# Kernel tuning notes

Hardware: AMD Instinct MI355X
Metric: run time of the kernel (lower is better)

## Reference

```python
import jax, jax.numpy as jnp
import numpy as np

H = 384
W = 384
C_X = 64       # channels of x (== out_channels)
C_PTX = 64     # channels of ptx
C_IN = C_X + C_PTX  # Linear in_channels = 128
C_OUT = 64
N_TGT = 120000  # number of target pixels (CSR segments)
DEG = 8         # points per target pixel
N_PTS = N_TGT * DEG


def setup_inputs() -> dict:
    key = jax.random.key(0)
    k1, k2, k3, k4 = jax.random.split(key, 4)
    x = jax.random.normal(k1, (1, C_X, H, W), jnp.float32)
    ptx = jax.random.normal(k2, (N_PTS, C_PTX), jnp.float32)
    # CSR row pointer over points per target pixel (monotone, ends at N_PTS)
    point_key = jnp.arange(N_TGT + 1, dtype=jnp.int32) * DEG
    # unique target-pixel indices into H*W
    pixel_tgt_idx = jnp.arange(N_TGT, dtype=jnp.int32)
    sm_w = jax.random.normal(k3, (C_IN, 1), jnp.float32) * 0.05
    sm_b = jnp.zeros((1,), jnp.float32)
    fo_w = jax.random.normal(k4, (C_IN, C_OUT), jnp.float32) * 0.05
    fo_b = jnp.zeros((C_OUT,), jnp.float32)
    return {"x": x, "ptx": ptx, "sm_w": sm_w, "sm_b": sm_b,
            "fo_w": fo_w, "fo_b": fo_b, "point_key": point_key,
            "pixel_tgt_idx": pixel_tgt_idx, "bs": 1, "height": H, "width": W}


def reference(x, ptx, sm_w, sm_b, fo_w, fo_b, point_key, pixel_tgt_idx, bs, height, width):
    # segment id per point from CSR rowptr (static total length for jit)
    seg = jnp.repeat(jnp.arange(N_TGT, dtype=jnp.int32), jnp.diff(point_key),
                     total_repeat_length=N_PTS)
    # pixel features gathered to target pixels, then CSR-gathered to points
    feat_px = x.transpose(0, 2, 3, 1).reshape(height * width, C_X)[pixel_tgt_idx]
    feat = jnp.concatenate([ptx, feat_px[seg]], axis=1)  # [N_PTS, C_IN]
    # _net_forward: identity (base class)
    # segment softmax over points within each pixel group
    logits = feat @ sm_w + sm_b  # [N_PTS, 1]
    m = jax.ops.segment_max(logits, seg, num_segments=N_TGT)
    e = jnp.exp(logits - m[seg])
    s = jax.ops.segment_sum(e, seg, num_segments=N_TGT)
    weight = e / (s[seg] + 1e-16)
    # feat_out projection replaces ptx
    ptx_out = feat @ fo_w + fo_b  # [N_PTS, C_OUT]
    agg = jax.ops.segment_sum(weight * ptx_out, seg, num_segments=N_TGT)  # [N_TGT, C_OUT]
    # list_to_map: scatter aggregated features back to image grid + mask
    flat = jnp.zeros((height * width, C_OUT), x.dtype).at[pixel_tgt_idx].set(agg)
    mask = jnp.zeros((height * width, 1), x.dtype).at[pixel_tgt_idx].set(1.0)
    fmap = flat.reshape(1, height, width, C_OUT).transpose(0, 3, 1, 2)
    mmap = mask.reshape(1, height, width, 1).transpose(0, 3, 1, 2)
    x_out = jnp.where(mmap > 0, fmap, x)
    return x_out, ptx_out
```

## Files before the change

### kernel.cpp

```cpp
#include <hip/hip_runtime.h>
#include <hip/hip_bf16.h>
#include <math.h>

typedef __attribute__((ext_vector_type(8))) short short8v;
typedef __attribute__((ext_vector_type(4))) float float4v;

#define TB 64

__device__ __forceinline__ short f2bf(float f) {
    __hip_bfloat16 h = __float2bfloat16(f);
    short s; __builtin_memcpy(&s, &h, sizeof(short));
    return s;
}
__device__ __forceinline__ float4v mfma_bf16(short8v a, short8v b, float4v c) {
    return __builtin_amdgcn_mfma_f32_16x16x32_bf16(a, b, c, 0, 0, 0);
}

__device__ __forceinline__ int WTI(int row, int col) {
    return row * 72 + (col ^ (((row >> 2) & 7) << 3));
}

__global__ __launch_bounds__(256)
void copy_x_kernel(const float4* __restrict__ x, float4* __restrict__ out, int n4) {
    int i = blockIdx.x * blockDim.x + threadIdx.x;
    if (i < n4) out[i] = x[i];
}

__global__ __launch_bounds__(256, 4)
void fused_kernel(const float* __restrict__ x,
                  const float* __restrict__ ptx,
                  const float* __restrict__ sm_w,
                  const float* __restrict__ fo_w,
                  const float* __restrict__ fo_b,
                  const int* __restrict__ point_key,
                  const int* __restrict__ pixel_tgt_idx,
                  float* __restrict__ xout,
                  float* __restrict__ ptx_out,
                  int n_tgt, int n_pts, int hw)
{
    __shared__ __align__(16) char sraw[34816];
    unsigned short (*fpx)[72] = (unsigned short (*)[72])sraw;
    unsigned short* wTf       = (unsigned short*)(sraw + 9216);
    float (*q_lds)[68]        = (float (*)[68])sraw;
    float (*agg)[68]          = (float (*)[68])(sraw + 17408);
    __shared__ int pix_s[TB], r0_s[TB], deg_s[TB];

    const int tid  = threadIdx.x;
    const int lane = tid & 63;
    const int w    = tid >> 6;
    const int lo16 = lane & 15;
    const int g    = lane >> 4;
    const int t0   = blockIdx.x * TB;
    const int tw0  = w * 16;

    float4 wv[8];
    {
        const float4* fw4 = (const float4*)fo_w;
        #pragma unroll
        for (int i = 0; i < 8; ++i) wv[i] = fw4[i * 256 + tid];
    }
    float4 fb40 = *(const float4*)&fo_b[ 0 + g * 4];
    float4 fb41 = *(const float4*)&fo_b[16 + g * 4];
    float4 fb42 = *(const float4*)&fo_b[32 + g * 4];
    float4 fb43 = *(const float4*)&fo_b[48 + g * 4];
    if (tid < TB) {
        int t = t0 + tid;
        bool v = t < n_tgt;
        int r0 = v ? point_key[t] : 0;
        int d  = v ? (point_key[t + 1] - r0) : 0;
        pix_s[tid] = v ? pixel_tgt_idx[t] : 0;
        r0_s[tid]  = r0;
        deg_s[tid] = d > 8 ? 8 : d;
    }

    #pragma unroll
    for (int i = 0; i < 8; ++i) {
        int flat = (i * 256 + tid) * 4;
        int k = flat >> 6, c = flat & 63;
        int wrow0 = (k & 64) + c;
        int col = k & 63;
        wTf[WTI(wrow0 + 0, col)] = (unsigned short)f2bf(wv[i].x);
        wTf[WTI(wrow0 + 1, col)] = (unsigned short)f2bf(wv[i].y);
        wTf[WTI(wrow0 + 2, col)] = (unsigned short)f2bf(wv[i].z);
        wTf[WTI(wrow0 + 3, col)] = (unsigned short)f2bf(wv[i].w);
    }
    __syncthreads();

    int pgm[8];
    #pragma unroll
    for (int mt = 0; mt < 8; ++mt) {
        int tlA = tw0 + mt * 2 + (lo16 >> 3);
        int pg  = r0_s[tlA] + (lo16 & 7);
        pgm[mt] = pg < n_pts ? pg : n_pts - 1;
    }

    {
        const int tgt = tid >> 2, q4 = tid & 3;
        const int pix = pix_s[tgt];
        const float* xp = x + (size_t)(q4 * 16) * hw + pix;
        #pragma unroll
        for (int hhalf = 0; hhalf < 2; ++hhalf) {
            short8v pk;
            #pragma unroll
            for (int j = 0; j < 8; ++j)
                pk[j] = f2bf(xp[(size_t)(hhalf * 8 + j) * hw]);
            *(short8v*)&fpx[tgt][q4 * 16 + hhalf * 8] = pk;
        }
    }

    short8v b1[5][2];
    #pragma unroll
    for (int ct = 0; ct < 4; ++ct)
        #pragma unroll
        for (int kh = 0; kh < 2; ++kh)
            b1[ct][kh] = *(const short8v*)&wTf[WTI(ct * 16 + lo16, kh * 32 + g * 8)];
    #pragma unroll
    for (int kh = 0; kh < 2; ++kh) {
        short8v bb;
        #pragma unroll
        for (int j = 0; j < 8; ++j)
            bb[j] = f2bf(sm_w[kh * 32 + g * 8 + j]);
        b1[4][kh] = bb;
    }

    float4 lb0, lb1, lb2, lb3;
    {
        const float* prow = ptx + (size_t)pgm[0] * 64 + g * 8;
        lb0 = *(const float4*)(prow);
        lb1 = *(const float4*)(prow + 4);
        lb2 = *(const float4*)(prow + 32);
        lb3 = *(const float4*)(prow + 36);
    }
    __syncthreads();

    float4v qv4[4];
    {
        short8v a20 = *(const short8v*)&fpx[tw0 + lo16][g * 8];
        short8v a21 = *(const short8v*)&fpx[tw0 + lo16][32 + g * 8];
        #pragma unroll
        for (int ct = 0; ct < 4; ++ct) {
            short8v b20 = *(const short8v*)&wTf[WTI(64 + ct * 16 + lo16, g * 8)];
            short8v b21 = *(const short8v*)&wTf[WTI(64 + ct * 16 + lo16, 32 + g * 8)];
            float4v z = {0.f, 0.f, 0.f, 0.f};
            z = mfma_bf16(b20, a20, z);
            qv4[ct] = mfma_bf16(b21, a21, z);
        }
    }
    __syncthreads();
    {
        float4v t0v = qv4[0]; t0v[0] += fb40.x; t0v[1] += fb40.y; t0v[2] += fb40.z; t0v[3] += fb40.w;
        float4v t1v = qv4[1]; t1v[0] += fb41.x; t1v[1] += fb41.y; t1v[2] += fb41.z; t1v[3] += fb41.w;
        float4v t2v = qv4[2]; t2v[0] += fb42.x; t2v[1] += fb42.y; t2v[2] += fb42.z; t2v[3] += fb42.w;
        float4v t3v = qv4[3]; t3v[0] += fb43.x; t3v[1] += fb43.y; t3v[2] += fb43.z; t3v[3] += fb43.w;
        *(float4v*)&q_lds[tw0 + lo16][ 0 + g * 4] = t0v;
        *(float4v*)&q_lds[tw0 + lo16][16 + g * 4] = t1v;
        *(float4v*)&q_lds[tw0 + lo16][32 + g * 4] = t2v;
        *(float4v*)&q_lds[tw0 + lo16][48 + g * 4] = t3v;
    }

#define EPIL_CT(CT, CREG)                                                      \
    {                                                                          \
        const int colb = (CT) * 16 + g * 4;                                    \
        const float4 q4 = *(const float4*)&q_lds[tE][colb];                    \
        float4v po;                                                            \
        po[0] = CREG[0] + q4.x; po[1] = CREG[1] + q4.y;                        \
        po[2] = CREG[2] + q4.z; po[3] = CREG[3] + q4.w;                        \
        if (val)                                                               \
            *(float4v*)&ptx_out[(size_t)(r0E + pE) * 64 + colb] = po;          \
        float s0 = po[0] * wn, s1 = po[1] * wn, s2 = po[2] * wn, s3 = po[3] * wn; \
        s0 += __shfl_xor(s0, 1); s1 += __shfl_xor(s1, 1);                      \
        s2 += __shfl_xor(s2, 1); s3 += __shfl_xor(s3, 1);                      \
        s0 += __shfl_xor(s0, 2); s1 += __shfl_xor(s1, 2);                      \
        s2 += __shfl_xor(s2, 2); s3 += __shfl_xor(s3, 2);                      \
        s0 += __shfl_xor(s0, 4); s1 += __shfl_xor(s1, 4);                      \
        s2 += __shfl_xor(s2, 4); s3 += __shfl_xor(s3, 4);                      \
        if (pE == 0) {                                                         \
            float4v ag; ag[0] = s0; ag[1] = s1; ag[2] = s2; ag[3] = s3;        \
            *(float4v*)&agg[tE][colb] = ag;                                    \
        }                                                                      \
    }

    #pragma unroll
    for (int mt = 0; mt < 8; ++mt) {
        short8v a0, a1;
        a0[0] = f2bf(lb0.x); a0[1] = f2bf(lb0.y); a0[2] = f2bf(lb0.z); a0[3] = f2bf(lb0.w);
        a0[4] = f2bf(lb1.x); a0[5] = f2bf(lb1.y); a0[6] = f2bf(lb1.z); a0[7] = f2bf(lb1.w);
        a1[0] = f2bf(lb2.x); a1[1] = f2bf(lb2.y); a1[2] = f2bf(lb2.z); a1[3] = f2bf(lb2.w);
        a1[4] = f2bf(lb3.x); a1[5] = f2bf(lb3.y); a1[6] = f2bf(lb3.z); a1[7] = f2bf(lb3.w);

        if (mt < 7) {
            const float* prow = ptx + (size_t)pgm[mt + 1] * 64 + g * 8;
            lb0 = *(const float4*)(prow);
            lb1 = *(const float4*)(prow + 4);
            lb2 = *(const float4*)(prow + 32);
            lb3 = *(const float4*)(prow + 36);
        }

        float4v z = {0.f, 0.f, 0.f, 0.f};
        float4v cc0 = mfma_bf16(b1[0][1], a1, mfma_bf16(b1[0][0], a0, z));
        float4v cc1 = mfma_bf16(b1[1][1], a1, mfma_bf16(b1[1][0], a0, z));
        float4v cc2 = mfma_bf16(b1[2][1], a1, mfma_bf16(b1[2][0], a0, z));
        float4v cc3 = mfma_bf16(b1[3][1], a1, mfma_bf16(b1[3][0], a0, z));
        float4v cc4 = mfma_bf16(b1[4][1], a1, mfma_bf16(b1[4][0], a0, z));

        const int tE   = tw0 + mt * 2 + (lo16 >> 3);
        const int degE = deg_s[tE];
        const int r0E  = r0_s[tE];
        const int pE   = lo16 & 7;
        const bool val = (pE < degE);

        float lg = val ? cc4[0] : -3.4e38f;
        float mx = lg;
        mx = fmaxf(mx, __shfl_xor(mx, 1));
        mx = fmaxf(mx, __shfl_xor(mx, 2));
        mx = fmaxf(mx, __shfl_xor(mx, 4));
        float e = val ? __expf(lg - mx) : 0.0f;
        float sm = e;
        sm += __shfl_xor(sm, 1);
        sm += __shfl_xor(sm, 2);
        sm += __shfl_xor(sm, 4);
        const float wn = e / (sm + 1e-16f);

        EPIL_CT(0, cc0)
        EPIL_CT(1, cc1)
        EPIL_CT(2, cc2)
        EPIL_CT(3, cc3)
    }
#undef EPIL_CT
    __syncthreads();

    {
        const int tgt = tid >> 2, q4 = tid & 3;
        if (t0 + tgt < n_tgt) {
            const int pix = pix_s[tgt];
            float* xp = xout + (size_t)(q4 * 16) * hw + pix;
            #pragma unroll
            for (int u = 0; u < 4; ++u) {
                float4 v = *(const float4*)&agg[tgt][q4 * 16 + u * 4];
                xp[(size_t)(u * 4 + 0) * hw] = v.x;
                xp[(size_t)(u * 4 + 1) * hw] = v.y;
                xp[(size_t)(u * 4 + 2) * hw] = v.z;
                xp[(size_t)(u * 4 + 3) * hw] = v.w;
            }
        }
    }
}

extern "C" void kernel_launch(void* const* d_in, const int* in_sizes, int n_in,
                              void* d_out, int out_size, void* d_ws, size_t ws_size,
                              hipStream_t stream) {
    const float* x             = (const float*)d_in[0];
    const float* ptx           = (const float*)d_in[1];
    const float* sm_w          = (const float*)d_in[2];
    const float* fo_w          = (const float*)d_in[4];
    const float* fo_b          = (const float*)d_in[5];
    const int*   point_key     = (const int*)d_in[6];
    const int*   pixel_tgt_idx = (const int*)d_in[7];

    const int x_elems = in_sizes[0];
    const int hw      = x_elems / 64;
    const int n_tgt   = in_sizes[7];
    const int n_pts   = in_sizes[1] / 64;

    float* xout    = (float*)d_out;
    float* ptx_out = xout + (size_t)x_elems;

    const int n4 = x_elems / 4;
    copy_x_kernel<<<(n4 + 255) / 256, 256, 0, stream>>>(
        (const float4*)x, (float4*)xout, n4);

    const int blocks = (n_tgt + TB - 1) / TB;
    fused_kernel<<<blocks, 256, 0, stream>>>(
        x, ptx, sm_w, fo_w, fo_b, point_key, pixel_tgt_idx,
        xout, ptx_out, n_tgt, n_pts, hw);
}
```

Baseline: 137.0 us.

## Skip copying masked x pixels, store q in bf16 LDS, deepen ptx prefetch

Builds a per-pixel byte mask of target pixels in workspace and copies only the groups of four pixels that are not fully covered by targets, so x rows overwritten by the fused kernel are not copied. The per-target q projection is stored in LDS as bf16 instead of fp32, which shrinks shared memory enough to raise launch bounds to 5 blocks per CU. The ptx row prefetch becomes two-deep. The bf16 q adds rounding error to ptx_out, and the extra memset and mask launches add fixed overhead.

New measurement: 254.0 us. 1.85x slower.

```diff
diff --git a/kernel.cpp b/kernel.cpp
--- a/kernel.cpp
+++ b/kernel.cpp
@@ -3,6 +3,7 @@
 #include <math.h>
 
 typedef __attribute__((ext_vector_type(8))) short short8v;
+typedef __attribute__((ext_vector_type(4))) short short4v;
 typedef __attribute__((ext_vector_type(4))) float float4v;
 
 #define TB 64
@@ -12,12 +13,33 @@
     short s; __builtin_memcpy(&s, &h, sizeof(short));
     return s;
 }
+__device__ __forceinline__ float bf2f(short u) {
+    unsigned int x = ((unsigned int)(unsigned short)u) << 16;
+    float f; __builtin_memcpy(&f, &x, sizeof(float));
+    return f;
+}
 __device__ __forceinline__ float4v mfma_bf16(short8v a, short8v b, float4v c) {
     return __builtin_amdgcn_mfma_f32_16x16x32_bf16(a, b, c, 0, 0, 0);
 }
 
 __device__ __forceinline__ int WTI(int row, int col) {
     return row * 72 + (col ^ (((row >> 2) & 7) << 3));
+}
+
+__global__ __launch_bounds__(256)
+void mask_set_kernel(const int* __restrict__ idx, unsigned char* __restrict__ mask, int n) {
+    int i = blockIdx.x * blockDim.x + threadIdx.x;
+    if (i < n) mask[idx[i]] = 1;
+}
+
+__global__ __launch_bounds__(256)
+void copy_masked_kernel(const float4* __restrict__ x, float4* __restrict__ out,
+                        const unsigned int* __restrict__ mask4, int q4n) {
+    int q = blockIdx.x * blockDim.x + threadIdx.x;
+    if (q >= q4n) return;
+    if (mask4[q] == 0x01010101u) return;
+    size_t idx = (size_t)blockIdx.y * q4n + q;
+    out[idx] = x[idx];
 }
 
 __global__ __launch_bounds__(256)
@@ -26,7 +48,7 @@
     if (i < n4) out[i] = x[i];
 }
 
-__global__ __launch_bounds__(256, 4)
+__global__ __launch_bounds__(256, 5)
 void fused_kernel(const float* __restrict__ x,
                   const float* __restrict__ ptx,
                   const float* __restrict__ sm_w,
@@ -38,11 +60,11 @@
                   float* __restrict__ ptx_out,
                   int n_tgt, int n_pts, int hw)
 {
-    __shared__ __align__(16) char sraw[34816];
-    unsigned short (*fpx)[72] = (unsigned short (*)[72])sraw;
-    unsigned short* wTf       = (unsigned short*)(sraw + 9216);
-    float (*q_lds)[68]        = (float (*)[68])sraw;
-    float (*agg)[68]          = (float (*)[68])(sraw + 17408);
+    __shared__ __align__(16) char sraw[27648];
+    unsigned short (*fpx)[72]   = (unsigned short (*)[72])sraw;
+    unsigned short* wTf         = (unsigned short*)(sraw + 9216);
+    unsigned short (*q_lds)[72] = (unsigned short (*)[72])sraw;
+    float (*agg)[68]            = (float (*)[68])(sraw + 9216);
     __shared__ int pix_s[TB], r0_s[TB], deg_s[TB];
 
     const int tid  = threadIdx.x;
@@ -94,6 +116,20 @@
         pgm[mt] = pg < n_pts ? pg : n_pts - 1;
     }
 
+    float4 cb0, cb1, cb2, cb3, nb0, nb1, nb2, nb3;
+    {
+        const float* prow = ptx + (size_t)pgm[0] * 64 + g * 8;
+        cb0 = *(const float4*)(prow);
+        cb1 = *(const float4*)(prow + 4);
+        cb2 = *(const float4*)(prow + 32);
+        cb3 = *(const float4*)(prow + 36);
+        const float* prow1 = ptx + (size_t)pgm[1] * 64 + g * 8;
+        nb0 = *(const float4*)(prow1);
+        nb1 = *(const float4*)(prow1 + 4);
+        nb2 = *(const float4*)(prow1 + 32);
+        nb3 = *(const float4*)(prow1 + 36);
+    }
+
     {
         const int tgt = tid >> 2, q4 = tid & 3;
         const int pix = pix_s[tgt];
@@ -122,15 +158,6 @@
             bb[j] = f2bf(sm_w[kh * 32 + g * 8 + j]);
         b1[4][kh] = bb;
     }
-
-    float4 lb0, lb1, lb2, lb3;
-    {
-        const float* prow = ptx + (size_t)pgm[0] * 64 + g * 8;
-        lb0 = *(const float4*)(prow);
-        lb1 = *(const float4*)(prow + 4);
-        lb2 = *(const float4*)(prow + 32);
-        lb3 = *(const float4*)(prow + 36);
-    }
     __syncthreads();
 
     float4v qv4[4];
@@ -148,23 +175,28 @@
     }
     __syncthreads();
     {
-        float4v t0v = qv4[0]; t0v[0] += fb40.x; t0v[1] += fb40.y; t0v[2] += fb40.z; t0v[3] += fb40.w;
-        float4v t1v = qv4[1]; t1v[0] += fb41.x; t1v[1] += fb41.y; t1v[2] += fb41.z; t1v[3] += fb41.w;
-        float4v t2v = qv4[2]; t2v[0] += fb42.x; t2v[1] += fb42.y; t2v[2] += fb42.z; t2v[3] += fb42.w;
-        float4v t3v = qv4[3]; t3v[0] += fb43.x; t3v[1] += fb43.y; t3v[2] += fb43.z; t3v[3] += fb43.w;
-        *(float4v*)&q_lds[tw0 + lo16][ 0 + g * 4] = t0v;
-        *(float4v*)&q_lds[tw0 + lo16][16 + g * 4] = t1v;
-        *(float4v*)&q_lds[tw0 + lo16][32 + g * 4] = t2v;
-        *(float4v*)&q_lds[tw0 + lo16][48 + g * 4] = t3v;
+        short4v q0, q1, q2, q3;
+        q0[0] = f2bf(qv4[0][0] + fb40.x); q0[1] = f2bf(qv4[0][1] + fb40.y);
+        q0[2] = f2bf(qv4[0][2] + fb40.z); q0[3] = f2bf(qv4[0][3] + fb40.w);
+        q1[0] = f2bf(qv4[1][0] + fb41.x); q1[1] = f2bf(qv4[1][1] + fb41.y);
+        q1[2] = f2bf(qv4[1][2] + fb41.z); q1[3] = f2bf(qv4[1][3] + fb41.w);
+        q2[0] = f2bf(qv4[2][0] + fb42.x); q2[1] = f2bf(qv4[2][1] + fb42.y);
+        q2[2] = f2bf(qv4[2][2] + fb42.z); q2[3] = f2bf(qv4[2][3] + fb42.w);
+        q3[0] = f2bf(qv4[3][0] + fb43.x); q3[1] = f2bf(qv4[3][1] + fb43.y);
+        q3[2] = f2bf(qv4[3][2] + fb43.z); q3[3] = f2bf(qv4[3][3] + fb43.w);
+        *(short4v*)&q_lds[tw0 + lo16][ 0 + g * 4] = q0;
+        *(short4v*)&q_lds[tw0 + lo16][16 + g * 4] = q1;
+        *(short4v*)&q_lds[tw0 + lo16][32 + g * 4] = q2;
+        *(short4v*)&q_lds[tw0 + lo16][48 + g * 4] = q3;
     }
 
 #define EPIL_CT(CT, CREG)                                                      \
     {                                                                          \
         const int colb = (CT) * 16 + g * 4;                                    \
-        const float4 q4 = *(const float4*)&q_lds[tE][colb];                    \
+        const short4v qb = *(const short4v*)&q_lds[tE][colb];                  \
         float4v po;                                                            \
-        po[0] = CREG[0] + q4.x; po[1] = CREG[1] + q4.y;                        \
-        po[2] = CREG[2] + q4.z; po[3] = CREG[3] + q4.w;                        \
+        po[0] = CREG[0] + bf2f(qb[0]); po[1] = CREG[1] + bf2f(qb[1]);          \
+        po[2] = CREG[2] + bf2f(qb[2]); po[3] = CREG[3] + bf2f(qb[3]);          \
         if (val)                                                               \
             *(float4v*)&ptx_out[(size_t)(r0E + pE) * 64 + colb] = po;          \
         float s0 = po[0] * wn, s1 = po[1] * wn, s2 = po[2] * wn, s3 = po[3] * wn; \
@@ -183,17 +215,18 @@
     #pragma unroll
     for (int mt = 0; mt < 8; ++mt) {
         short8v a0, a1;
-        a0[0] = f2bf(lb0.x); a0[1] = f2bf(lb0.y); a0[2] = f2bf(lb0.z); a0[3] = f2bf(lb0.w);
-        a0[4] = f2bf(lb1.x); a0[5] = f2bf(lb1.y); a0[6] = f2bf(lb1.z); a0[7] = f2bf(lb1.w);
-        a1[0] = f2bf(lb2.x); a1[1] = f2bf(lb2.y); a1[2] = f2bf(lb2.z); a1[3] = f2bf(lb2.w);
-        a1[4] = f2bf(lb3.x); a1[5] = f2bf(lb3.y); a1[6] = f2bf(lb3.z); a1[7] = f2bf(lb3.w);
-
-        if (mt < 7) {
-            const float* prow = ptx + (size_t)pgm[mt + 1] * 64 + g * 8;
-            lb0 = *(const float4*)(prow);
-            lb1 = *(const float4*)(prow + 4);
-            lb2 = *(const float4*)(prow + 32);
-            lb3 = *(const float4*)(prow + 36);
+        a0[0] = f2bf(cb0.x); a0[1] = f2bf(cb0.y); a0[2] = f2bf(cb0.z); a0[3] = f2bf(cb0.w);
+        a0[4] = f2bf(cb1.x); a0[5] = f2bf(cb1.y); a0[6] = f2bf(cb1.z); a0[7] = f2bf(cb1.w);
+        a1[0] = f2bf(cb2.x); a1[1] = f2bf(cb2.y); a1[2] = f2bf(cb2.z); a1[3] = f2bf(cb2.w);
+        a1[4] = f2bf(cb3.x); a1[5] = f2bf(cb3.y); a1[6] = f2bf(cb3.z); a1[7] = f2bf(cb3.w);
+
+        cb0 = nb0; cb1 = nb1; cb2 = nb2; cb3 = nb3;
+        if (mt < 6) {
+            const float* prow = ptx + (size_t)pgm[mt + 2] * 64 + g * 8;
+            nb0 = *(const float4*)(prow);
+            nb1 = *(const float4*)(prow + 4);
+            nb2 = *(const float4*)(prow + 32);
+            nb3 = *(const float4*)(prow + 36);
         }
 
         float4v z = {0.f, 0.f, 0.f, 0.f};
@@ -265,9 +298,19 @@
     float* xout    = (float*)d_out;
     float* ptx_out = xout + (size_t)x_elems;
 
-    const int n4 = x_elems / 4;
-    copy_x_kernel<<<(n4 + 255) / 256, 256, 0, stream>>>(
-        (const float4*)x, (float4*)xout, n4);
+    if (ws_size >= (size_t)hw && (hw & 3) == 0) {
+        hipMemsetAsync(d_ws, 0, (size_t)hw, stream);
+        mask_set_kernel<<<(n_tgt + 255) / 256, 256, 0, stream>>>(
+            pixel_tgt_idx, (unsigned char*)d_ws, n_tgt);
+        const int q4n = hw / 4;
+        dim3 cgrid((q4n + 255) / 256, 64);
+        copy_masked_kernel<<<cgrid, 256, 0, stream>>>(
+            (const float4*)x, (float4*)xout, (const unsigned int*)d_ws, q4n);
+    } else {
+        const int n4 = x_elems / 4;
+        copy_x_kernel<<<(n4 + 255) / 256, 256, 0, stream>>>(
+            (const float4*)x, (float4*)xout, n4);
+    }
 
     const int blocks = (n_tgt + TB - 1) / TB;
     fused_kernel<<<blocks, 256, 0, stream>>>(
```
